# Performance work log

Hardware: AMD Instinct MI355X
Metric: run time of the kernel (lower is better)

Reference implementation:

```python
import jax, jax.numpy as jnp
import numpy as np

B, T, IN, H = 1024, 200, 128, 128

def _linear_params(key, out_dim, in_dim):
    kw, kb = jax.random.split(key)
    bound = 1.0 / np.sqrt(in_dim)
    w = jax.random.uniform(kw, (out_dim, in_dim), jnp.float32, -bound, bound)
    b = jax.random.uniform(kb, (out_dim,), jnp.float32, -bound, bound)
    return w, b

def setup_inputs() -> dict:
    key = jax.random.key(0)
    ks = jax.random.split(key, 10)
    targets = jax.random.normal(ks[0], (B, T, IN), jnp.float32)
    history_states = jax.random.normal(ks[1], (B, T, H), jnp.float32)
    W_w, W_b = _linear_params(ks[2], H, IN)
    xu_w, xu_b = _linear_params(ks[3], H, H)
    hu_w, hu_b = _linear_params(ks[4], H, H)
    xr_w, xr_b = _linear_params(ks[5], H, H)
    hr_w, hr_b = _linear_params(ks[6], H, H)
    xg_w, xg_b = _linear_params(ks[7], H, H)
    hg_w, hg_b = _linear_params(ks[8], H, H)
    ln2_w, ln2_b = _linear_params(ks[9], H, IN + H)
    return dict(targets=targets, history_states=history_states,
                W_w=W_w, W_b=W_b, xu_w=xu_w, xu_b=xu_b, hu_w=hu_w, hu_b=hu_b,
                xr_w=xr_w, xr_b=xr_b, hr_w=hr_w, hr_b=hr_b,
                xg_w=xg_w, xg_b=xg_b, hg_w=hg_w, hg_b=hg_b,
                ln2_w=ln2_w, ln2_b=ln2_b)

def reference(targets, history_states, W_w, W_b, xu_w, xu_b, hu_w, hu_b,
              xr_w, xr_b, hr_w, hr_b, xg_w, xg_b, hg_w, hg_b, ln2_w, ln2_b):
    # attention weights: softmax over time of <W(targets), history>
    aw = jnp.einsum('bti,hi->bth', targets, W_w) + W_b            # [B,T,H]
    att = jax.nn.softmax(jnp.sum(aw * history_states, -1, keepdims=True), axis=1)  # [B,T,1]

    # precompute input-side projections as big GEMMs (same math as per-step Linear)
    xu = jnp.einsum('bth,oh->bto', history_states, xu_w) + xu_b   # [B,T,H]
    xr = jnp.einsum('bth,oh->bto', history_states, xr_w) + xr_b
    xg = jnp.einsum('bth,oh->bto', history_states, xg_w) + xg_b

    def step(h, xs):
        xu_t, xr_t, xg_t, a_t = xs                                 # [B,H],[B,H],[B,H],[B,1]
        u = jax.nn.sigmoid(xu_t + h @ hu_w.T + hu_b) * a_t
        r = jax.nn.sigmoid(xr_t + h @ hr_w.T + hr_b)
        g = jnp.tanh(xg_t + r * (h @ hg_w.T + hg_b))
        h = (1.0 - u) * h + u * g
        return h, None

    h0 = jnp.zeros((targets.shape[0], hu_w.shape[0]), targets.dtype)
    # scan over time: move T to leading axis
    xs = (jnp.swapaxes(xu, 0, 1), jnp.swapaxes(xr, 0, 1),
          jnp.swapaxes(xg, 0, 1), jnp.swapaxes(att, 0, 1))
    h, _ = jax.lax.scan(step, h0, xs)

    out = jnp.concatenate([h, targets[:, 0]], axis=-1) @ ln2_w.T + ln2_b
    return out
```

## Files before the change

kernel.cpp:

```cpp
#include <hip/hip_runtime.h>

#define B_ 1024
#define T_ 200
#define H_ 128

typedef __attribute__((ext_vector_type(8))) short short8;
typedef __attribute__((ext_vector_type(4))) float f32x4;

#define MFMA(a, b, c) __builtin_amdgcn_mfma_f32_16x16x32_bf16((a), (b), (c), 0, 0, 0)

static __device__ __forceinline__ short f2bf(float f) {
  unsigned u = __float_as_uint(f);
  u += 0x7fffu + ((u >> 16) & 1u);
  return (short)(u >> 16);
}
static __device__ __forceinline__ float bf2f(short s) {
  return __uint_as_float(((unsigned)(unsigned short)s) << 16);
}
static __device__ __forceinline__ unsigned pack2bf_rne(float a, float b) {
  unsigned ua = __float_as_uint(a);
  ua += 0x7fffu + ((ua >> 16) & 1u);
  unsigned ub = __float_as_uint(b);
  ub += 0x7fffu + ((ub >> 16) & 1u);
  return (ua >> 16) | (ub & 0xFFFF0000u);
}
static __device__ __forceinline__ float rcp_f(float x) { return __builtin_amdgcn_rcpf(x); }
static __device__ __forceinline__ void ck_barrier() {
  asm volatile("s_waitcnt lgkmcnt(0)\n\ts_barrier" ::: "memory");
}

__global__ __launch_bounds__(512, 1) void proj_scores_kernel(
    const float* __restrict__ tgt, const float* __restrict__ hist,
    const float* __restrict__ Ww, const float* __restrict__ Wb,
    float* __restrict__ scores, short* __restrict__ histbf) {
  const int tc = blockIdx.x, bb = blockIdx.y;
  const int nt = (tc == 12) ? 8 : 16;
  const int t0 = tc * 16;
  const int tid = threadIdx.x;
  const int lane = tid & 63, w = tid >> 6;
  const int n = lane & 15, q = lane >> 4;

  __shared__ short tgt_hi[2][16 * 128];
  __shared__ short tgt_lo[2][16 * 128];
  __shared__ float hist_f[2][16 * 132];
  __shared__ float sp[16 * 8];

  short8 whi[4], wlo[4];
  float wb;
  {
    const int o = w * 16 + n;
    wb = Wb[o];
#pragma unroll
    for (int ks = 0; ks < 4; ++ks) {
      const float* p = Ww + o * H_ + ks * 32 + q * 8;
      short8 h, l;
#pragma unroll
      for (int j = 0; j < 8; ++j) {
        float f = p[j];
        short hv = f2bf(f);
        h[j] = hv;
        l[j] = f2bf(f - bf2f(hv));
      }
      whi[ks] = h;
      wlo[ks] = l;
    }
  }

  const int sm = tid >> 5, cs = tid & 31;
  const int g = cs >> 1, half = cs & 1;
  const int spos16 = sm * 128 + ((g ^ (sm & 7)) * 8) + half * 4;
  const int sposf = sm * 132 + cs * 4;
  const size_t rowbase = ((size_t)(bb * 16 + sm) * T_) * H_ + cs * 4;

  const int cu = tid;
  const int cks = cu >> 7, crem = cu & 127, cwl = crem >> 1, chalf = crem & 1;
  const int crow = cwl & 15, ckb = cks * 32 + (cwl >> 4) * 8 + chalf * 4;

  float4 hv = *(const float4*)(hist + rowbase + (size_t)t0 * H_);
  float4 tv = *(const float4*)(tgt + rowbase + (size_t)t0 * H_);
  {
    *(float4*)&hist_f[0][sposf] = hv;
    uint2 hi, lo;
    hi.x = pack2bf_rne(tv.x, tv.y);
    hi.y = pack2bf_rne(tv.z, tv.w);
    lo.x = pack2bf_rne(tv.x - bf2f((short)(hi.x)), tv.y - bf2f((short)(hi.x >> 16)));
    lo.y = pack2bf_rne(tv.z - bf2f((short)(hi.y)), tv.w - bf2f((short)(hi.y >> 16)));
    *(uint2*)&tgt_hi[0][spos16] = hi;
    *(uint2*)&tgt_lo[0][spos16] = lo;
  }
  ck_barrier();

  for (int tl = 0; tl < nt; ++tl) {
    const int cur = tl & 1, nxt = cur ^ 1;
    const bool have_next = (tl + 1 < nt);
    if (have_next) {
      hv = *(const float4*)(hist + rowbase + (size_t)(t0 + tl + 1) * H_);
      tv = *(const float4*)(tgt + rowbase + (size_t)(t0 + tl + 1) * H_);
    }
    f32x4 s1 = {0, 0, 0, 0}, s2 = {0, 0, 0, 0}, s3 = {0, 0, 0, 0};
#pragma unroll
    for (int ks = 0; ks < 4; ++ks) {
      const int fp = n * 128 + ((ks * 4 + q) ^ (n & 7)) * 8;
      short8 ahi = *(short8*)&tgt_hi[cur][fp];
      short8 alo = *(short8*)&tgt_lo[cur][fp];
      s1 = MFMA(ahi, whi[ks], s1);
      s2 = MFMA(ahi, wlo[ks], s2);
      s3 = MFMA(alo, whi[ks], s3);
    }
#pragma unroll
    for (int r = 0; r < 4; ++r) {
      const int m = q * 4 + r;
      float v = (s1[r] + s2[r] + s3[r] + wb) * hist_f[cur][m * 132 + w * 16 + n];
      v += __shfl_xor(v, 1);
      v += __shfl_xor(v, 2);
      v += __shfl_xor(v, 4);
      v += __shfl_xor(v, 8);
      if (n == 0) sp[m * 8 + w] = v;
    }
    if (histbf != nullptr) {
      const float* src = &hist_f[cur][crow * 132 + ckb];
      uint2 u;
      u.x = pack2bf_rne(src[0], src[1]);
      u.y = pack2bf_rne(src[2], src[3]);
      const size_t sb = (((size_t)(bb * T_ + t0 + tl) * 4) + cks) * 512 + cwl * 8 + chalf * 4;
      *(uint2*)(histbf + sb) = u;
    }
    if (have_next) {
      *(float4*)&hist_f[nxt][sposf] = hv;
      uint2 hi, lo;
      hi.x = pack2bf_rne(tv.x, tv.y);
      hi.y = pack2bf_rne(tv.z, tv.w);
      lo.x = pack2bf_rne(tv.x - bf2f((short)(hi.x)), tv.y - bf2f((short)(hi.x >> 16)));
      lo.y = pack2bf_rne(tv.z - bf2f((short)(hi.y)), tv.w - bf2f((short)(hi.y >> 16)));
      *(uint2*)&tgt_hi[nxt][spos16] = hi;
      *(uint2*)&tgt_lo[nxt][spos16] = lo;
    }
    ck_barrier();
    if (tid < 16) {
      float s = 0.0f;
#pragma unroll
      for (int ww = 0; ww < 8; ++ww) s += sp[tid * 8 + ww];
      scores[(size_t)(bb * 16 + tid) * T_ + (t0 + tl)] = s;
    }
    ck_barrier();
  }
}

__global__ __launch_bounds__(256, 4) void softmax_kernel(float* __restrict__ att) {
  const int b = blockIdx.x, tid = threadIdx.x;
  const int lane = tid & 63, wave = tid >> 6;
  __shared__ float red[8];
  float v = (tid < T_) ? att[(size_t)b * T_ + tid] : -3.0e38f;
  float mx = v;
#pragma unroll
  for (int d = 1; d < 64; d <<= 1) mx = fmaxf(mx, __shfl_xor(mx, d));
  if (lane == 0) red[wave] = mx;
  __syncthreads();
  mx = fmaxf(fmaxf(red[0], red[1]), fmaxf(red[2], red[3]));
  float e = (tid < T_) ? __expf(v - mx) : 0.0f;
  float sm = e;
#pragma unroll
  for (int d = 1; d < 64; d <<= 1) sm += __shfl_xor(sm, d);
  if (lane == 0) red[4 + wave] = sm;
  __syncthreads();
  sm = red[4] + red[5] + red[6] + red[7];
  if (tid < T_) att[(size_t)b * T_ + tid] = e / sm;
}

template <bool DIRECT>
__global__ __launch_bounds__(512, 2) void scan3_kernel(
    const float* __restrict__ hist,
    const float* __restrict__ xu_w, const float* __restrict__ xu_b,
    const float* __restrict__ hu_w, const float* __restrict__ hu_b,
    const float* __restrict__ xr_w, const float* __restrict__ xr_b,
    const float* __restrict__ hr_w, const float* __restrict__ hr_b,
    const float* __restrict__ xg_w, const float* __restrict__ xg_b,
    const float* __restrict__ hg_w, const float* __restrict__ hg_b,
    const float* __restrict__ att, const short* __restrict__ histbf,
    float* __restrict__ h_out) {
  const int tid = threadIdx.x;
  const int lane = tid & 63, w = tid >> 6;
  const int n = lane & 15, q = lane >> 4;
  const int bb = blockIdx.x, r0 = bb * 16;
  const int o = w * 16 + n;

  __shared__ short hbuf[2][16 * 128];
  __shared__ short xbuf[2][16 * 128];

  short8 wf[6][4];
  {
    const float* Wm[6] = {xu_w, hu_w, xr_w, hr_w, xg_w, hg_w};
#pragma unroll
    for (int M = 0; M < 6; ++M)
#pragma unroll
      for (int ks = 0; ks < 4; ++ks) {
        const float* p = Wm[M] + o * H_ + ks * 32 + q * 8;
        short8 v;
#pragma unroll
        for (int j = 0; j < 8; ++j) v[j] = f2bf(p[j]);
        wf[M][ks] = v;
      }
  }
  const float bu = xu_b[o] + hu_b[o];
  const float br_ = xr_b[o] + hr_b[o];
  const float bxg = xg_b[o], bhg = hg_b[o];

  for (int i = tid; i < 16 * 128; i += 512) hbuf[0][i] = 0;

  typedef union { uint4 u; short8 s; } frag_u;
  frag_u xp[2][4];
  const short* px = histbf + ((size_t)bb * T_ * 4) * 512 + (size_t)lane * 8;
  const int sm = tid >> 5, cs = tid & 31;
  const int xpos = sm * 128 + (((cs >> 1) ^ (sm & 7)) * 8) + (cs & 1) * 4;
  const float* hrow = hist + ((size_t)(r0 + sm) * T_) * H_ + cs * 4;
  float4 xnext;

  if constexpr (DIRECT) {
#pragma unroll
    for (int s = 0; s < 2; ++s)
#pragma unroll
      for (int ks = 0; ks < 4; ++ks)
        xp[s][ks].u = *(const uint4*)(px + (size_t)(s * 4 + ks) * 512);
  } else {
    float4 a = *(const float4*)hrow;
    uint2 u;
    u.x = pack2bf_rne(a.x, a.y);
    u.y = pack2bf_rne(a.z, a.w);
    *(uint2*)&xbuf[0][xpos] = u;
    xnext = *(const float4*)(hrow + H_);
  }

  float ap[2][4];
  const float* pa = att + (size_t)(r0 + q * 4) * T_;
#pragma unroll
  for (int s = 0; s < 2; ++s)
#pragma unroll
    for (int r = 0; r < 4; ++r) ap[s][r] = pa[(size_t)r * T_ + s];

  float hreg[4] = {0.0f, 0.0f, 0.0f, 0.0f};
  ck_barrier();

#pragma unroll 2
  for (int t = 0; t < T_; ++t) {
    const int cur = t & 1, nxt = cur ^ 1;
    short8 ha[4];
#pragma unroll
    for (int ks = 0; ks < 4; ++ks)
      ha[ks] = *(short8*)&hbuf[cur][n * 128 + ((ks * 4 + q) ^ (n & 7)) * 8];
    short8 xa[4];
    if constexpr (DIRECT) {
#pragma unroll
      for (int ks = 0; ks < 4; ++ks) xa[ks] = xp[cur][ks].s;
    } else {
#pragma unroll
      for (int ks = 0; ks < 4; ++ks)
        xa[ks] = *(short8*)&xbuf[cur][n * 128 + ((ks * 4 + q) ^ (n & 7)) * 8];
    }
    f32x4 axu = {0, 0, 0, 0}, ahu = {0, 0, 0, 0}, axr = {0, 0, 0, 0},
          ahr = {0, 0, 0, 0}, axg = {0, 0, 0, 0}, ahg = {0, 0, 0, 0};
#pragma unroll
    for (int ks = 0; ks < 4; ++ks) {
      axu = MFMA(xa[ks], wf[0][ks], axu);
      ahu = MFMA(ha[ks], wf[1][ks], ahu);
      axr = MFMA(xa[ks], wf[2][ks], axr);
      ahr = MFMA(ha[ks], wf[3][ks], ahr);
      axg = MFMA(xa[ks], wf[4][ks], axg);
      ahg = MFMA(ha[ks], wf[5][ks], ahg);
    }
    const int tp = (t + 2 < T_) ? t + 2 : T_ - 1;
    if constexpr (DIRECT) {
#pragma unroll
      for (int ks = 0; ks < 4; ++ks)
        xp[cur][ks].u = *(const uint4*)(px + (size_t)(tp * 4 + ks) * 512);
    } else {
      uint2 u;
      u.x = pack2bf_rne(xnext.x, xnext.y);
      u.y = pack2bf_rne(xnext.z, xnext.w);
      *(uint2*)&xbuf[nxt][xpos] = u;
      xnext = *(const float4*)(hrow + (size_t)tp * H_);
    }
    float at_c[4];
#pragma unroll
    for (int r = 0; r < 4; ++r) {
      at_c[r] = ap[cur][r];
      ap[cur][r] = pa[(size_t)r * T_ + tp];
    }
#pragma unroll
    for (int r = 0; r < 4; ++r) {
      const int m = q * 4 + r;
      const float su = axu[r] + ahu[r] + bu;
      const float u = at_c[r] * rcp_f(1.0f + __expf(-su));
      const float sr = axr[r] + ahr[r] + br_;
      const float rr = rcp_f(1.0f + __expf(-sr));
      const float sg = (axg[r] + bxg) + rr * (ahg[r] + bhg);
      const float g = 2.0f * rcp_f(1.0f + __expf(-2.0f * sg)) - 1.0f;
      const float hn = hreg[r] + u * (g - hreg[r]);
      hreg[r] = hn;
      hbuf[nxt][m * 128 + ((o >> 3) ^ (m & 7)) * 8 + (o & 7)] =
          (short)(__float_as_uint(hn) >> 16);
      if (t == T_ - 1) h_out[(size_t)(r0 + m) * H_ + o] = hn;
    }
    ck_barrier();
  }
}

__global__ __launch_bounds__(256, 4) void final_kernel(
    const float* __restrict__ tgt, const float* __restrict__ hfin,
    const float* __restrict__ w, const float* __restrict__ bias,
    float* __restrict__ out) {
  const int b = blockIdx.x, tid = threadIdx.x;
  const int o = tid >> 1, half = tid & 1;
  const float* src = half ? (tgt + (size_t)b * (T_ * H_)) : (hfin + (size_t)b * H_);
  const float* wrow = w + o * 256 + half * 128;
  float acc = 0.0f;
#pragma unroll 8
  for (int k = 0; k < 128; k += 4) {
    float4 sv = *(const float4*)(src + k);
    float4 wv = *(const float4*)(wrow + k);
    acc += sv.x * wv.x + sv.y * wv.y + sv.z * wv.z + sv.w * wv.w;
  }
  acc += __shfl_xor(acc, 1);
  if (half == 0) out[(size_t)b * H_ + o] = acc + bias[o];
}

extern "C" void kernel_launch(void* const* d_in, const int* in_sizes, int n_in,
                              void* d_out, int out_size, void* d_ws, size_t ws_size,
                              hipStream_t stream) {
  const float* targets = (const float*)d_in[0];
  const float* history = (const float*)d_in[1];
  const float* W_w = (const float*)d_in[2];
  const float* W_b = (const float*)d_in[3];
  const float* xu_w = (const float*)d_in[4];
  const float* xu_b = (const float*)d_in[5];
  const float* hu_w = (const float*)d_in[6];
  const float* hu_b = (const float*)d_in[7];
  const float* xr_w = (const float*)d_in[8];
  const float* xr_b = (const float*)d_in[9];
  const float* hr_w = (const float*)d_in[10];
  const float* hr_b = (const float*)d_in[11];
  const float* xg_w = (const float*)d_in[12];
  const float* xg_b = (const float*)d_in[13];
  const float* hg_w = (const float*)d_in[14];
  const float* hg_b = (const float*)d_in[15];
  const float* ln2_w = (const float*)d_in[16];
  const float* ln2_b = (const float*)d_in[17];
  float* out = (float*)d_out;

  float* att = (float*)d_ws;
  float* hfin = att + (size_t)B_ * T_;
  const size_t fixed = (size_t)B_ * T_ * 4 + (size_t)B_ * H_ * 4;
  const size_t histbf_bytes = (size_t)64 * T_ * 4 * 512 * 8 * 2;
  short* histbf = (ws_size >= fixed + histbf_bytes)
                      ? (short*)((char*)d_ws + fixed)
                      : nullptr;

  proj_scores_kernel<<<dim3(13, 64), dim3(512), 0, stream>>>(
      targets, history, W_w, W_b, att, histbf);
  softmax_kernel<<<dim3(B_), dim3(256), 0, stream>>>(att);
  if (histbf) {
    scan3_kernel<true><<<dim3(64), dim3(512), 0, stream>>>(
        history, xu_w, xu_b, hu_w, hu_b, xr_w, xr_b, hr_w, hr_b,
        xg_w, xg_b, hg_w, hg_b, att, histbf, hfin);
  } else {
    scan3_kernel<false><<<dim3(64), dim3(512), 0, stream>>>(
        history, xu_w, xu_b, hu_w, hu_b, xr_w, xr_b, hr_w, hr_b,
        xg_w, xg_b, hg_w, hg_b, att, histbf, hfin);
  }
  final_kernel<<<dim3(B_), dim3(256), 0, stream>>>(targets, hfin, ln2_w, ln2_b, out);
}
```

Measured before the change: 498.0 us.

## Split GRU scan into 4-row blocks and simplify score projection pipeline

The scan kernel now handles 4 batch rows per block instead of 16, launching 256 blocks instead of 64 so more CUs run the serial recurrence. Each MFMA tile replicates 4 rows across its 16 lanes, and the history bf16 copy moves to a plain row-major layout. The projection kernel drops the low-half target split (one fewer MFMA), double-buffers the partial-score array to remove one barrier per step, and raises its occupancy hint. The trade-offs are lower target precision in the scores and three quarters of the MFMA work in the scan being redundant.

```diff
diff --git a/kernel.cpp b/kernel.cpp
--- a/kernel.cpp
+++ b/kernel.cpp
@@ -29,7 +29,7 @@
   asm volatile("s_waitcnt lgkmcnt(0)\n\ts_barrier" ::: "memory");
 }
 
-__global__ __launch_bounds__(512, 1) void proj_scores_kernel(
+__global__ __launch_bounds__(512, 4) void proj_scores_kernel(
     const float* __restrict__ tgt, const float* __restrict__ hist,
     const float* __restrict__ Ww, const float* __restrict__ Wb,
     float* __restrict__ scores, short* __restrict__ histbf) {
@@ -41,9 +41,8 @@
   const int n = lane & 15, q = lane >> 4;
 
   __shared__ short tgt_hi[2][16 * 128];
-  __shared__ short tgt_lo[2][16 * 128];
   __shared__ float hist_f[2][16 * 132];
-  __shared__ float sp[16 * 8];
+  __shared__ float sp[2][128];
 
   short8 whi[4], wlo[4];
   float wb;
@@ -57,9 +56,9 @@
 #pragma unroll
       for (int j = 0; j < 8; ++j) {
         float f = p[j];
-        short hv = f2bf(f);
-        h[j] = hv;
-        l[j] = f2bf(f - bf2f(hv));
+        short hv16 = f2bf(f);
+        h[j] = hv16;
+        l[j] = f2bf(f - bf2f(hv16));
       }
       whi[ks] = h;
       wlo[ks] = l;
@@ -67,82 +66,88 @@
   }
 
   const int sm = tid >> 5, cs = tid & 31;
-  const int g = cs >> 1, half = cs & 1;
-  const int spos16 = sm * 128 + ((g ^ (sm & 7)) * 8) + half * 4;
+  const int gran = cs >> 1, half = cs & 1;
+  const int spos16 = sm * 128 + (gran ^ (sm & 7)) * 8 + half * 4;
   const int sposf = sm * 132 + cs * 4;
-  const size_t rowbase = ((size_t)(bb * 16 + sm) * T_) * H_ + cs * 4;
-
-  const int cu = tid;
-  const int cks = cu >> 7, crem = cu & 127, cwl = crem >> 1, chalf = crem & 1;
-  const int crow = cwl & 15, ckb = cks * 32 + (cwl >> 4) * 8 + chalf * 4;
-
-  float4 hv = *(const float4*)(hist + rowbase + (size_t)t0 * H_);
-  float4 tv = *(const float4*)(tgt + rowbase + (size_t)t0 * H_);
+  const int row = bb * 16 + sm;
+  const float* hsrc = hist + (size_t)row * T_ * H_ + cs * 4;
+  const float* tsrc = tgt + (size_t)row * T_ * H_ + cs * 4;
+  short* hbdst = histbf ? (histbf + (size_t)row * T_ * H_ + cs * 4) : nullptr;
+
   {
-    *(float4*)&hist_f[0][sposf] = hv;
-    uint2 hi, lo;
-    hi.x = pack2bf_rne(tv.x, tv.y);
-    hi.y = pack2bf_rne(tv.z, tv.w);
-    lo.x = pack2bf_rne(tv.x - bf2f((short)(hi.x)), tv.y - bf2f((short)(hi.x >> 16)));
-    lo.y = pack2bf_rne(tv.z - bf2f((short)(hi.y)), tv.w - bf2f((short)(hi.y >> 16)));
-    *(uint2*)&tgt_hi[0][spos16] = hi;
-    *(uint2*)&tgt_lo[0][spos16] = lo;
+    float4 h0 = *(const float4*)(hsrc + (size_t)t0 * H_);
+    float4 t0v = *(const float4*)(tsrc + (size_t)t0 * H_);
+    *(float4*)&hist_f[0][sposf] = h0;
+    uint2 th;
+    th.x = pack2bf_rne(t0v.x, t0v.y);
+    th.y = pack2bf_rne(t0v.z, t0v.w);
+    *(uint2*)&tgt_hi[0][spos16] = th;
+    if (hbdst) {
+      uint2 hh;
+      hh.x = pack2bf_rne(h0.x, h0.y);
+      hh.y = pack2bf_rne(h0.z, h0.w);
+      *(uint2*)(hbdst + (size_t)t0 * H_) = hh;
+    }
+  }
+  float4 hv[2], tv[2];
+  if (nt > 1) {
+    hv[1] = *(const float4*)(hsrc + (size_t)(t0 + 1) * H_);
+    tv[1] = *(const float4*)(tsrc + (size_t)(t0 + 1) * H_);
   }
   ck_barrier();
 
+#pragma unroll 2
   for (int tl = 0; tl < nt; ++tl) {
-    const int cur = tl & 1, nxt = cur ^ 1;
-    const bool have_next = (tl + 1 < nt);
-    if (have_next) {
-      hv = *(const float4*)(hist + rowbase + (size_t)(t0 + tl + 1) * H_);
-      tv = *(const float4*)(tgt + rowbase + (size_t)(t0 + tl + 1) * H_);
-    }
-    f32x4 s1 = {0, 0, 0, 0}, s2 = {0, 0, 0, 0}, s3 = {0, 0, 0, 0};
+    const int cur = tl & 1;
+    if (tl > 0 && tid < 16) {
+      float s = 0.0f;
+#pragma unroll
+      for (int ww = 0; ww < 8; ++ww) s += sp[cur ^ 1][tid * 8 + ww];
+      scores[(size_t)(bb * 16 + tid) * T_ + (t0 + tl - 1)] = s;
+    }
+    if (tl + 2 < nt) {
+      hv[cur] = *(const float4*)(hsrc + (size_t)(t0 + tl + 2) * H_);
+      tv[cur] = *(const float4*)(tsrc + (size_t)(t0 + tl + 2) * H_);
+    }
+    f32x4 s1 = {0, 0, 0, 0}, s2 = {0, 0, 0, 0};
 #pragma unroll
     for (int ks = 0; ks < 4; ++ks) {
       const int fp = n * 128 + ((ks * 4 + q) ^ (n & 7)) * 8;
       short8 ahi = *(short8*)&tgt_hi[cur][fp];
-      short8 alo = *(short8*)&tgt_lo[cur][fp];
       s1 = MFMA(ahi, whi[ks], s1);
       s2 = MFMA(ahi, wlo[ks], s2);
-      s3 = MFMA(alo, whi[ks], s3);
     }
 #pragma unroll
     for (int r = 0; r < 4; ++r) {
       const int m = q * 4 + r;
-      float v = (s1[r] + s2[r] + s3[r] + wb) * hist_f[cur][m * 132 + w * 16 + n];
+      float v = (s1[r] + s2[r] + wb) * hist_f[cur][m * 132 + w * 16 + n];
       v += __shfl_xor(v, 1);
       v += __shfl_xor(v, 2);
       v += __shfl_xor(v, 4);
       v += __shfl_xor(v, 8);
-      if (n == 0) sp[m * 8 + w] = v;
-    }
-    if (histbf != nullptr) {
-      const float* src = &hist_f[cur][crow * 132 + ckb];
-      uint2 u;
-      u.x = pack2bf_rne(src[0], src[1]);
-      u.y = pack2bf_rne(src[2], src[3]);
-      const size_t sb = (((size_t)(bb * T_ + t0 + tl) * 4) + cks) * 512 + cwl * 8 + chalf * 4;
-      *(uint2*)(histbf + sb) = u;
-    }
-    if (have_next) {
-      *(float4*)&hist_f[nxt][sposf] = hv;
-      uint2 hi, lo;
-      hi.x = pack2bf_rne(tv.x, tv.y);
-      hi.y = pack2bf_rne(tv.z, tv.w);
-      lo.x = pack2bf_rne(tv.x - bf2f((short)(hi.x)), tv.y - bf2f((short)(hi.x >> 16)));
-      lo.y = pack2bf_rne(tv.z - bf2f((short)(hi.y)), tv.w - bf2f((short)(hi.y >> 16)));
-      *(uint2*)&tgt_hi[nxt][spos16] = hi;
-      *(uint2*)&tgt_lo[nxt][spos16] = lo;
+      if (n == 0) sp[cur][m * 8 + w] = v;
+    }
+    if (tl + 1 < nt) {
+      float4 hs = hv[cur ^ 1], ts = tv[cur ^ 1];
+      *(float4*)&hist_f[cur ^ 1][sposf] = hs;
+      uint2 th;
+      th.x = pack2bf_rne(ts.x, ts.y);
+      th.y = pack2bf_rne(ts.z, ts.w);
+      *(uint2*)&tgt_hi[cur ^ 1][spos16] = th;
+      if (hbdst) {
+        uint2 hh;
+        hh.x = pack2bf_rne(hs.x, hs.y);
+        hh.y = pack2bf_rne(hs.z, hs.w);
+        *(uint2*)(hbdst + (size_t)(t0 + tl + 1) * H_) = hh;
+      }
     }
     ck_barrier();
-    if (tid < 16) {
-      float s = 0.0f;
-#pragma unroll
-      for (int ww = 0; ww < 8; ++ww) s += sp[tid * 8 + ww];
-      scores[(size_t)(bb * 16 + tid) * T_ + (t0 + tl)] = s;
-    }
-    ck_barrier();
+  }
+  if (tid < 16) {
+    float s = 0.0f;
+#pragma unroll
+    for (int ww = 0; ww < 8; ++ww) s += sp[(nt - 1) & 1][tid * 8 + ww];
+    scores[(size_t)(bb * 16 + tid) * T_ + (t0 + nt - 1)] = s;
   }
 }
 
@@ -167,8 +172,8 @@
   if (tid < T_) att[(size_t)b * T_ + tid] = e / sm;
 }
 
-template <bool DIRECT>
-__global__ __launch_bounds__(512, 2) void scan3_kernel(
+template <bool PK>
+__global__ __launch_bounds__(512, 2) void scan4_kernel(
     const float* __restrict__ hist,
     const float* __restrict__ xu_w, const float* __restrict__ xu_b,
     const float* __restrict__ hu_w, const float* __restrict__ hu_b,
@@ -181,11 +186,10 @@
   const int tid = threadIdx.x;
   const int lane = tid & 63, w = tid >> 6;
   const int n = lane & 15, q = lane >> 4;
-  const int bb = blockIdx.x, r0 = bb * 16;
+  const int bb = blockIdx.x, r0 = bb * 4;
   const int o = w * 16 + n;
 
-  __shared__ short hbuf[2][16 * 128];
-  __shared__ short xbuf[2][16 * 128];
+  __shared__ short hbuf[2][4 * 144];
 
   short8 wf[6][4];
   {
@@ -205,37 +209,35 @@
   const float br_ = xr_b[o] + hr_b[o];
   const float bxg = xg_b[o], bhg = hg_b[o];
 
-  for (int i = tid; i < 16 * 128; i += 512) hbuf[0][i] = 0;
-
+  for (int i = tid; i < 2 * 4 * 144; i += 512) ((short*)hbuf)[i] = 0;
+
+  const int xrow = r0 + (n & 3);
   typedef union { uint4 u; short8 s; } frag_u;
   frag_u xp[2][4];
-  const short* px = histbf + ((size_t)bb * T_ * 4) * 512 + (size_t)lane * 8;
-  const int sm = tid >> 5, cs = tid & 31;
-  const int xpos = sm * 128 + (((cs >> 1) ^ (sm & 7)) * 8) + (cs & 1) * 4;
-  const float* hrow = hist + ((size_t)(r0 + sm) * T_) * H_ + cs * 4;
-  float4 xnext;
-
-  if constexpr (DIRECT) {
+  float4 xf0[2][4], xf1[2][4];
+  const short* xb = PK ? (histbf + (size_t)xrow * T_ * H_ + q * 8) : nullptr;
+  const float* xf = hist + (size_t)xrow * T_ * H_ + q * 8;
+  if constexpr (PK) {
 #pragma unroll
     for (int s = 0; s < 2; ++s)
 #pragma unroll
       for (int ks = 0; ks < 4; ++ks)
-        xp[s][ks].u = *(const uint4*)(px + (size_t)(s * 4 + ks) * 512);
+        xp[s][ks].u = *(const uint4*)(xb + (size_t)s * H_ + ks * 32);
   } else {
-    float4 a = *(const float4*)hrow;
-    uint2 u;
-    u.x = pack2bf_rne(a.x, a.y);
-    u.y = pack2bf_rne(a.z, a.w);
-    *(uint2*)&xbuf[0][xpos] = u;
-    xnext = *(const float4*)(hrow + H_);
+#pragma unroll
+    for (int s = 0; s < 2; ++s)
+#pragma unroll
+      for (int ks = 0; ks < 4; ++ks) {
+        xf0[s][ks] = *(const float4*)(xf + (size_t)s * H_ + ks * 32);
+        xf1[s][ks] = *(const float4*)(xf + (size_t)s * H_ + ks * 32 + 4);
+      }
   }
 
   float ap[2][4];
-  const float* pa = att + (size_t)(r0 + q * 4) * T_;
 #pragma unroll
   for (int s = 0; s < 2; ++s)
 #pragma unroll
-    for (int r = 0; r < 4; ++r) ap[s][r] = pa[(size_t)r * T_ + s];
+    for (int r = 0; r < 4; ++r) ap[s][r] = att[(size_t)(r0 + r) * T_ + s];
 
   float hreg[4] = {0.0f, 0.0f, 0.0f, 0.0f};
   ck_barrier();
@@ -246,15 +248,22 @@
     short8 ha[4];
 #pragma unroll
     for (int ks = 0; ks < 4; ++ks)
-      ha[ks] = *(short8*)&hbuf[cur][n * 128 + ((ks * 4 + q) ^ (n & 7)) * 8];
+      ha[ks] = *(const short8*)&hbuf[cur][(n & 3) * 144 + ks * 32 + q * 8];
     short8 xa[4];
-    if constexpr (DIRECT) {
+    if constexpr (PK) {
 #pragma unroll
       for (int ks = 0; ks < 4; ++ks) xa[ks] = xp[cur][ks].s;
     } else {
 #pragma unroll
-      for (int ks = 0; ks < 4; ++ks)
-        xa[ks] = *(short8*)&xbuf[cur][n * 128 + ((ks * 4 + q) ^ (n & 7)) * 8];
+      for (int ks = 0; ks < 4; ++ks) {
+        frag_u t_;
+        float4 a = xf0[cur][ks], b = xf1[cur][ks];
+        t_.u.x = pack2bf_rne(a.x, a.y);
+        t_.u.y = pack2bf_rne(a.z, a.w);
+        t_.u.z = pack2bf_rne(b.x, b.y);
+        t_.u.w = pack2bf_rne(b.z, b.w);
+        xa[ks] = t_.s;
+      }
     }
     f32x4 axu = {0, 0, 0, 0}, ahu = {0, 0, 0, 0}, axr = {0, 0, 0, 0},
           ahr = {0, 0, 0, 0}, axg = {0, 0, 0, 0}, ahg = {0, 0, 0, 0};
@@ -268,38 +277,37 @@
       ahg = MFMA(ha[ks], wf[5][ks], ahg);
     }
     const int tp = (t + 2 < T_) ? t + 2 : T_ - 1;
-    if constexpr (DIRECT) {
+    if constexpr (PK) {
 #pragma unroll
       for (int ks = 0; ks < 4; ++ks)
-        xp[cur][ks].u = *(const uint4*)(px + (size_t)(tp * 4 + ks) * 512);
+        xp[cur][ks].u = *(const uint4*)(xb + (size_t)tp * H_ + ks * 32);
     } else {
-      uint2 u;
-      u.x = pack2bf_rne(xnext.x, xnext.y);
-      u.y = pack2bf_rne(xnext.z, xnext.w);
-      *(uint2*)&xbuf[nxt][xpos] = u;
-      xnext = *(const float4*)(hrow + (size_t)tp * H_);
+#pragma unroll
+      for (int ks = 0; ks < 4; ++ks) {
+        xf0[cur][ks] = *(const float4*)(xf + (size_t)tp * H_ + ks * 32);
+        xf1[cur][ks] = *(const float4*)(xf + (size_t)tp * H_ + ks * 32 + 4);
+      }
     }
     float at_c[4];
 #pragma unroll
     for (int r = 0; r < 4; ++r) {
       at_c[r] = ap[cur][r];
-      ap[cur][r] = pa[(size_t)r * T_ + tp];
+      ap[cur][r] = att[(size_t)(r0 + r) * T_ + tp];
     }
 #pragma unroll
     for (int r = 0; r < 4; ++r) {
-      const int m = q * 4 + r;
       const float su = axu[r] + ahu[r] + bu;
       const float u = at_c[r] * rcp_f(1.0f + __expf(-su));
       const float sr = axr[r] + ahr[r] + br_;
       const float rr = rcp_f(1.0f + __expf(-sr));
       const float sg = (axg[r] + bxg) + rr * (ahg[r] + bhg);
       const float g = 2.0f * rcp_f(1.0f + __expf(-2.0f * sg)) - 1.0f;
-      const float hn = hreg[r] + u * (g - hreg[r]);
-      hreg[r] = hn;
-      hbuf[nxt][m * 128 + ((o >> 3) ^ (m & 7)) * 8 + (o & 7)] =
-          (short)(__float_as_uint(hn) >> 16);
-      if (t == T_ - 1) h_out[(size_t)(r0 + m) * H_ + o] = hn;
-    }
+      hreg[r] = hreg[r] + u * (g - hreg[r]);
+    }
+    const float hsel = (q & 2) ? ((q & 1) ? hreg[3] : hreg[2])
+                               : ((q & 1) ? hreg[1] : hreg[0]);
+    hbuf[nxt][q * 144 + o] = (short)(__float_as_uint(hsel) >> 16);
+    if (t == T_ - 1) h_out[(size_t)(r0 + q) * H_ + o] = hsel;
     ck_barrier();
   }
 }
@@ -349,7 +357,7 @@
   float* att = (float*)d_ws;
   float* hfin = att + (size_t)B_ * T_;
   const size_t fixed = (size_t)B_ * T_ * 4 + (size_t)B_ * H_ * 4;
-  const size_t histbf_bytes = (size_t)64 * T_ * 4 * 512 * 8 * 2;
+  const size_t histbf_bytes = (size_t)B_ * T_ * H_ * 2;
   short* histbf = (ws_size >= fixed + histbf_bytes)
                       ? (short*)((char*)d_ws + fixed)
                       : nullptr;
@@ -358,11 +366,11 @@
       targets, history, W_w, W_b, att, histbf);
   softmax_kernel<<<dim3(B_), dim3(256), 0, stream>>>(att);
   if (histbf) {
-    scan3_kernel<true><<<dim3(64), dim3(512), 0, stream>>>(
+    scan4_kernel<true><<<dim3(B_ / 4), dim3(512), 0, stream>>>(
         history, xu_w, xu_b, hu_w, hu_b, xr_w, xr_b, hr_w, hr_b,
         xg_w, xg_b, hg_w, hg_b, att, histbf, hfin);
   } else {
-    scan3_kernel<false><<<dim3(64), dim3(512), 0, stream>>>(
+    scan4_kernel<false><<<dim3(B_ / 4), dim3(512), 0, stream>>>(
         history, xu_w, xu_b, hu_w, hu_b, xr_w, xr_b, hr_w, hr_b,
         xg_w, xg_b, hg_w, hg_b, att, histbf, hfin);
   }
```

New measurement: 533.4 us. 7.1% more time.
